# Performance work log

Measured on AMD Instinct MI355X. Metric: run time of the kernel, lower is better.

Reference implementation:

```python
import jax, jax.numpy as jnp
from jax import lax
import numpy as np

P, K1, K2 = 8, 5, 9  # nPaths, small/large ECA kernel sizes (from nDim=1024, nPaths=8)
LN_EPS = 1e-5


def setup_inputs() -> dict:
    key = jax.random.key(0)
    ks = jax.random.split(key, 6)
    b, c, l = 16, 1024, 4096
    return {
        "x": jax.random.normal(ks[0], (b, c, l), dtype=jnp.float32),
        "conv1_w": jax.random.normal(ks[1], (P, K1), dtype=jnp.float32) * 0.3,
        "conv2_w": jax.random.normal(ks[2], (P, K2), dtype=jnp.float32) * 0.3,
        "combine_w": jax.random.normal(ks[3], (2,), dtype=jnp.float32) * 0.5,
        "combine_b": jnp.zeros((), dtype=jnp.float32),
        "ln_g": jnp.ones((P,), dtype=jnp.float32),
        "ln_b": jnp.zeros((P,), dtype=jnp.float32),
        "W1": jax.random.normal(ks[4], (P, 2 * P), dtype=jnp.float32) * 0.3,
        "b1": jnp.zeros((2 * P,), dtype=jnp.float32),
        "W2": jax.random.normal(ks[5], (2 * P, P), dtype=jnp.float32) * 0.3,
        "b2": jnp.zeros((P,), dtype=jnp.float32),
    }


def _grouped_conv(y, w):
    # y: (b, P, D) pooled per-path features; w: (P, k) one 1-ch kernel per path.
    # Equivalent to the per-path Conv1d(1,1,k, padding=(k-1)//2) loop, fused.
    k = w.shape[-1]
    pad = (k - 1) // 2
    return lax.conv_general_dilated(
        y, w[:, None, :], window_strides=(1,), padding=[(pad, pad)],
        dimension_numbers=("NCH", "OIH", "NCH"), feature_group_count=y.shape[1])


def reference(x, conv1_w, conv2_w, combine_w, combine_b, ln_g, ln_b, W1, b1, W2, b2):
    b, c, l = x.shape
    nP = conv1_w.shape[0]
    D = c // nP
    pf = x.reshape(b, nP, D, l)          # (b, P, D, l)
    y = pf.mean(-1)                      # (b, P, D) global-avg-pool over l
    y1 = _grouped_conv(y, conv1_w)       # (b, P, D)
    y2 = _grouped_conv(y, conv2_w)       # (b, P, D)
    # combine = Conv1d(2,1,1): scalar mix of the two conv outputs + bias
    attn = jax.nn.sigmoid(combine_w[0] * y1 + combine_w[1] * y2 + combine_b)
    # cross-path gating MLP on per-path mean attention
    cross = attn.mean(-1)                # (b, P)
    mu = cross.mean(-1, keepdims=True)
    var = cross.var(-1, keepdims=True)   # biased, matches torch LayerNorm
    h = (cross - mu) / jnp.sqrt(var + LN_EPS) * ln_g + ln_b
    h = jax.nn.gelu(h @ W1 + b1, approximate=False)
    gate = jax.nn.sigmoid(h @ W2 + b2)   # (b, P)
    scale = attn * gate[:, :, None]      # (b, P, D)
    out = pf * scale[..., None]          # broadcast over l
    return out.reshape(b, c, l)
```

## Files before the change

kernel.cpp:

```cpp
#include <hip/hip_runtime.h>
#include <math.h>

#define NP 8
#define ND 128
#define NC 1024
#define NL 4096
#define NB 16
#define LN_EPS 1e-5f

#define NBLK 2048
#define RPB 8

typedef float v4f __attribute__((ext_vector_type(4)));

__device__ __forceinline__ float hsum(v4f v) { return v.x + v.y + v.z + v.w; }

__device__ __forceinline__ float gelu_f(float s) {
    const float t = 0.7978845608028654f * (s + 0.044715f * s * s * s);
    const float e = expf(2.f * t);
    return 0.5f * s * (1.f + (e - 1.f) / (e + 1.f));
}

__device__ __forceinline__ void gate_math(const float* __restrict__ scross,
                                          float* __restrict__ sgate,
                                          const float* ln_g, const float* ln_b,
                                          const float* W1, const float* b1,
                                          const float* W2, const float* b2) {
    float cross[NP];
    #pragma unroll
    for (int pp = 0; pp < NP; ++pp) cross[pp] = scross[pp];
    float mu = 0.f;
    #pragma unroll
    for (int pp = 0; pp < NP; ++pp) mu += cross[pp];
    mu *= (1.f / NP);
    float var = 0.f;
    #pragma unroll
    for (int pp = 0; pp < NP; ++pp) { float dl = cross[pp] - mu; var += dl * dl; }
    var *= (1.f / NP);
    const float inv = rsqrtf(var + LN_EPS);
    float h[NP];
    #pragma unroll
    for (int pp = 0; pp < NP; ++pp)
        h[pp] = (cross[pp] - mu) * inv * ln_g[pp] + ln_b[pp];
    float h2[2 * NP];
    for (int j = 0; j < 2 * NP; ++j) {
        float s = b1[j];
        #pragma unroll
        for (int pp = 0; pp < NP; ++pp) s += h[pp] * W1[pp * (2 * NP) + j];
        h2[j] = gelu_f(s);
    }
    for (int pp = 0; pp < NP; ++pp) {
        float s = b2[pp];
        #pragma unroll
        for (int j = 0; j < 2 * NP; ++j) s += h2[j] * W2[j * NP + pp];
        sgate[pp] = 1.f / (1.f + expf(-s));
    }
}

__device__ __forceinline__ void attn_math(const float* __restrict__ sy,
                                          float* __restrict__ sattn,
                                          const float* conv1_w, const float* conv2_w,
                                          const float* combine_w, const float* combine_b,
                                          int tid) {
    #pragma unroll
    for (int k = 0; k < 4; ++k) {
        const int pos = tid + 256 * k;
        const int p = pos >> 7, d = pos & 127;
        const float* rowp = sy + p * ND;
        float c1 = 0.f;
        #pragma unroll
        for (int t = 0; t < 5; ++t) {
            int dd = d + t - 2;
            float v = (dd >= 0 && dd < ND) ? rowp[dd] : 0.f;
            c1 += conv1_w[p * 5 + t] * v;
        }
        float c2 = 0.f;
        #pragma unroll
        for (int t = 0; t < 9; ++t) {
            int dd = d + t - 4;
            float v = (dd >= 0 && dd < ND) ? rowp[dd] : 0.f;
            c2 += conv2_w[p * 9 + t] * v;
        }
        const float z = combine_w[0] * c1 + combine_w[1] * c2 + combine_b[0];
        sattn[pos] = 1.f / (1.f + expf(-z));
    }
}

#define DECL_ROW(r) v4f xr##r##_0, xr##r##_1, xr##r##_2, xr##r##_3;
#define LOAD_ROW(r) { \
    const v4f* rp = xb + (size_t)(r) * (NL / 4); \
    xr##r##_0 = rp[tid]; xr##r##_1 = rp[tid + 256]; \
    xr##r##_2 = rp[tid + 512]; xr##r##_3 = rp[tid + 768]; \
    float ps = hsum(xr##r##_0) + hsum(xr##r##_1) + hsum(xr##r##_2) + hsum(xr##r##_3); \
    ps += __shfl_down(ps, 32, 64); ps += __shfl_down(ps, 16, 64); \
    ps += __shfl_down(ps, 8, 64);  ps += __shfl_down(ps, 4, 64); \
    ps += __shfl_down(ps, 2, 64);  ps += __shfl_down(ps, 1, 64); \
    if ((tid & 63) == 0) sred[r][tid >> 6] = ps; }
#define STORE_ROW(r) { \
    const float s = sattn[cbase + (r)] * g; \
    v4f* op = ob + (size_t)(r) * (NL / 4); \
    __builtin_nontemporal_store(xr##r##_0 * s, &op[tid]); \
    __builtin_nontemporal_store(xr##r##_1 * s, &op[tid + 256]); \
    __builtin_nontemporal_store(xr##r##_2 * s, &op[tid + 512]); \
    __builtin_nontemporal_store(xr##r##_3 * s, &op[tid + 768]); }

__global__ __launch_bounds__(256, 8) void fused_kernel(
    const float* __restrict__ x, float* __restrict__ y, unsigned* __restrict__ cnt,
    const float* __restrict__ conv1_w, const float* __restrict__ conv2_w,
    const float* __restrict__ combine_w, const float* __restrict__ combine_b,
    const float* __restrict__ ln_g, const float* __restrict__ ln_b,
    const float* __restrict__ W1, const float* __restrict__ b1,
    const float* __restrict__ W2, const float* __restrict__ b2,
    float* __restrict__ out)
{
    const int tid   = threadIdx.x;
    const int row0  = blockIdx.x * RPB;
    const int b     = row0 >> 10;
    const int cbase = row0 & (NC - 1);
    const int p0    = cbase >> 7;

    __shared__ float sred[RPB][4];
    __shared__ float sy[NC];
    __shared__ float sattn[NC];
    __shared__ float scross[NP];
    __shared__ float sgate[NP];

    const v4f* xb = (const v4f*)x + (size_t)row0 * (NL / 4);
    v4f* ob       = (v4f*)out    + (size_t)row0 * (NL / 4);

    DECL_ROW(0) DECL_ROW(1) DECL_ROW(2) DECL_ROW(3)
    DECL_ROW(4) DECL_ROW(5) DECL_ROW(6) DECL_ROW(7)

    LOAD_ROW(0) LOAD_ROW(1) LOAD_ROW(2) LOAD_ROW(3)
    LOAD_ROW(4) LOAD_ROW(5) LOAD_ROW(6) LOAD_ROW(7)
    __syncthreads();
    if (tid < RPB)
        y[row0 + tid] = (sred[tid][0] + sred[tid][1] + sred[tid][2] + sred[tid][3]) * (1.f / NL);
    __threadfence();
    __syncthreads();

    if (tid == 0) {
        __hip_atomic_fetch_add(cnt, 1u, __ATOMIC_RELEASE, __HIP_MEMORY_SCOPE_AGENT);
        while (__hip_atomic_load(cnt, __ATOMIC_ACQUIRE, __HIP_MEMORY_SCOPE_AGENT) < (unsigned)NBLK)
            __builtin_amdgcn_s_sleep(2);
    }
    __syncthreads();

    #pragma unroll
    for (int k = 0; k < 4; ++k) {
        const int i = tid + 256 * k;
        sy[i] = __hip_atomic_load(&y[b * NC + i], __ATOMIC_RELAXED, __HIP_MEMORY_SCOPE_AGENT);
    }
    __syncthreads();
    attn_math(sy, sattn, conv1_w, conv2_w, combine_w, combine_b, tid);
    __syncthreads();
    if (tid < 128) {
        const int p = tid >> 4, o = (tid & 15) * 8;
        float s = 0.f;
        #pragma unroll
        for (int j = 0; j < 8; ++j) s += sattn[p * ND + o + j];
        s += __shfl_down(s, 8, 16); s += __shfl_down(s, 4, 16);
        s += __shfl_down(s, 2, 16); s += __shfl_down(s, 1, 16);
        if ((tid & 15) == 0) scross[p] = s * (1.f / ND);
    }
    __syncthreads();
    if (tid == 0) gate_math(scross, sgate, ln_g, ln_b, W1, b1, W2, b2);
    __syncthreads();

    const float g = sgate[p0];
    STORE_ROW(0) STORE_ROW(1) STORE_ROW(2) STORE_ROW(3)
    STORE_ROW(4) STORE_ROW(5) STORE_ROW(6) STORE_ROW(7)
}

__global__ __launch_bounds__(256) void pool_kernel(const float* __restrict__ x,
                                                   float* __restrict__ y) {
    const int wid  = threadIdx.x >> 6;
    const int lane = threadIdx.x & 63;
    const int row  = blockIdx.x * 4 + wid;
    const v4f* xr = (const v4f*)(x + (size_t)row * NL);
    float s = 0.f;
    #pragma unroll
    for (int i = 0; i < 16; ++i) {
        v4f v = xr[lane + i * 64];
        s += v.x + v.y + v.z + v.w;
    }
    #pragma unroll
    for (int off = 32; off; off >>= 1) s += __shfl_down(s, off, 64);
    if (lane == 0) y[row] = s * (1.f / NL);
}

__global__ __launch_bounds__(1024) void attn_kernel(
    const float* __restrict__ y,
    const float* __restrict__ conv1_w, const float* __restrict__ conv2_w,
    const float* __restrict__ combine_w, const float* __restrict__ combine_b,
    const float* __restrict__ ln_g, const float* __restrict__ ln_b,
    const float* __restrict__ W1, const float* __restrict__ b1,
    const float* __restrict__ W2, const float* __restrict__ b2,
    float* __restrict__ scale)
{
    const int b = blockIdx.x;
    const int tid = threadIdx.x;
    const int p = tid >> 7;
    const int d = tid & 127;

    __shared__ float sy[NC];
    __shared__ float sattn[NC];
    __shared__ float sred[16];
    __shared__ float sgate[NP];

    sy[tid] = y[b * NC + tid];
    __syncthreads();

    const float* rowp = sy + p * ND;
    float c1 = 0.f;
    #pragma unroll
    for (int t = 0; t < 5; ++t) {
        int dd = d + t - 2;
        float v = (dd >= 0 && dd < ND) ? rowp[dd] : 0.f;
        c1 += conv1_w[p * 5 + t] * v;
    }
    float c2 = 0.f;
    #pragma unroll
    for (int t = 0; t < 9; ++t) {
        int dd = d + t - 4;
        float v = (dd >= 0 && dd < ND) ? rowp[dd] : 0.f;
        c2 += conv2_w[p * 9 + t] * v;
    }
    const float z = combine_w[0] * c1 + combine_w[1] * c2 + combine_b[0];
    const float a = 1.f / (1.f + expf(-z));
    sattn[tid] = a;

    float r = a;
    #pragma unroll
    for (int off = 32; off; off >>= 1) r += __shfl_down(r, off, 64);
    const int lane = tid & 63, wid = tid >> 6;
    if (lane == 0) sred[wid] = r;
    __syncthreads();

    if (tid == 0) {
        float scross[NP];
        #pragma unroll
        for (int pp = 0; pp < NP; ++pp)
            scross[pp] = (sred[2 * pp] + sred[2 * pp + 1]) * (1.f / ND);
        gate_math(scross, sgate, ln_g, ln_b, W1, b1, W2, b2);
    }
    __syncthreads();

    scale[b * NC + tid] = sattn[tid] * sgate[p];
}

__global__ __launch_bounds__(256) void scale_kernel(const float* __restrict__ x,
                                                    const float* __restrict__ scale,
                                                    float* __restrict__ out) {
    const v4f* xv = (const v4f*)x;
    v4f* ov = (v4f*)out;
    const size_t n = (size_t)NB * NC * (NL / 4);
    const size_t stride = (size_t)gridDim.x * blockDim.x;
    for (size_t i = (size_t)blockIdx.x * blockDim.x + threadIdx.x; i < n; i += stride) {
        const float s = scale[i >> 10];
        v4f v = xv[i];
        v *= s;
        __builtin_nontemporal_store(v, &ov[i]);
    }
}

extern "C" void kernel_launch(void* const* d_in, const int* in_sizes, int n_in,
                              void* d_out, int out_size, void* d_ws, size_t ws_size,
                              hipStream_t stream) {
    const float* x         = (const float*)d_in[0];
    const float* conv1_w   = (const float*)d_in[1];
    const float* conv2_w   = (const float*)d_in[2];
    const float* combine_w = (const float*)d_in[3];
    const float* combine_b = (const float*)d_in[4];
    const float* ln_g      = (const float*)d_in[5];
    const float* ln_b      = (const float*)d_in[6];
    const float* W1        = (const float*)d_in[7];
    const float* b1        = (const float*)d_in[8];
    const float* W2        = (const float*)d_in[9];
    const float* b2        = (const float*)d_in[10];
    float* out = (float*)d_out;

    float* y        = (float*)d_ws;
    float* scale    = y + NB * NC;
    unsigned* cnt   = (unsigned*)scale;

    hipMemsetAsync((void*)cnt, 0, 64, stream);

    int nb = 0;
    hipOccupancyMaxActiveBlocksPerMultiprocessor(&nb, fused_kernel, 256, 0);
    if (nb >= NBLK / 256) {
        void* args[] = { (void*)&x, (void*)&y, (void*)&cnt,
                         (void*)&conv1_w, (void*)&conv2_w,
                         (void*)&combine_w, (void*)&combine_b,
                         (void*)&ln_g, (void*)&ln_b,
                         (void*)&W1, (void*)&b1, (void*)&W2, (void*)&b2,
                         (void*)&out };
        hipLaunchCooperativeKernel((const void*)fused_kernel, dim3(NBLK), dim3(256),
                                   args, 0, stream);
    } else {
        pool_kernel<<<NB * NC / 4, 256, 0, stream>>>(x, y);
        attn_kernel<<<NB, 1024, 0, stream>>>(y, conv1_w, conv2_w, combine_w, combine_b,
                                             ln_g, ln_b, W1, b1, W2, b2, scale);
        scale_kernel<<<2048, 256, 0, stream>>>(x, scale, out);
    }
}
```

Baseline: 137.1 us.

## Process rows in chunks with a hierarchical per-chunk grid barrier

The fused cooperative kernel used to load 8 rows per block into registers and wait at a single grid-wide barrier on one counter. It now processes one row per block per chunk over 8 chunks. Each chunk runs a two-level barrier: 64 group counters feed a root counter, which cuts contention on one atomic. The gate MLP is also spread across threads instead of running serially on thread 0. The trade-off is 8 barrier round-trips and 8 recomputations of the attention and gate per block instead of one, and a batch's output now waits on barriers across all chunks.

```diff
diff --git a/kernel.cpp b/kernel.cpp
--- a/kernel.cpp
+++ b/kernel.cpp
@@ -9,11 +9,13 @@
 #define LN_EPS 1e-5f
 
 #define NBLK 2048
-#define RPB 8
+#define NCHUNK 8
+#define GRPS 64
 
 typedef float v4f __attribute__((ext_vector_type(4)));
 
 __device__ __forceinline__ float hsum(v4f v) { return v.x + v.y + v.z + v.w; }
+__device__ __forceinline__ float sigmoid_f(float z) { return 1.f / (1.f + expf(-z)); }
 
 __device__ __forceinline__ float gelu_f(float s) {
     const float t = 0.7978845608028654f * (s + 0.044715f * s * s * s);
@@ -21,91 +23,9 @@
     return 0.5f * s * (1.f + (e - 1.f) / (e + 1.f));
 }
 
-__device__ __forceinline__ void gate_math(const float* __restrict__ scross,
-                                          float* __restrict__ sgate,
-                                          const float* ln_g, const float* ln_b,
-                                          const float* W1, const float* b1,
-                                          const float* W2, const float* b2) {
-    float cross[NP];
-    #pragma unroll
-    for (int pp = 0; pp < NP; ++pp) cross[pp] = scross[pp];
-    float mu = 0.f;
-    #pragma unroll
-    for (int pp = 0; pp < NP; ++pp) mu += cross[pp];
-    mu *= (1.f / NP);
-    float var = 0.f;
-    #pragma unroll
-    for (int pp = 0; pp < NP; ++pp) { float dl = cross[pp] - mu; var += dl * dl; }
-    var *= (1.f / NP);
-    const float inv = rsqrtf(var + LN_EPS);
-    float h[NP];
-    #pragma unroll
-    for (int pp = 0; pp < NP; ++pp)
-        h[pp] = (cross[pp] - mu) * inv * ln_g[pp] + ln_b[pp];
-    float h2[2 * NP];
-    for (int j = 0; j < 2 * NP; ++j) {
-        float s = b1[j];
-        #pragma unroll
-        for (int pp = 0; pp < NP; ++pp) s += h[pp] * W1[pp * (2 * NP) + j];
-        h2[j] = gelu_f(s);
-    }
-    for (int pp = 0; pp < NP; ++pp) {
-        float s = b2[pp];
-        #pragma unroll
-        for (int j = 0; j < 2 * NP; ++j) s += h2[j] * W2[j * NP + pp];
-        sgate[pp] = 1.f / (1.f + expf(-s));
-    }
-}
-
-__device__ __forceinline__ void attn_math(const float* __restrict__ sy,
-                                          float* __restrict__ sattn,
-                                          const float* conv1_w, const float* conv2_w,
-                                          const float* combine_w, const float* combine_b,
-                                          int tid) {
-    #pragma unroll
-    for (int k = 0; k < 4; ++k) {
-        const int pos = tid + 256 * k;
-        const int p = pos >> 7, d = pos & 127;
-        const float* rowp = sy + p * ND;
-        float c1 = 0.f;
-        #pragma unroll
-        for (int t = 0; t < 5; ++t) {
-            int dd = d + t - 2;
-            float v = (dd >= 0 && dd < ND) ? rowp[dd] : 0.f;
-            c1 += conv1_w[p * 5 + t] * v;
-        }
-        float c2 = 0.f;
-        #pragma unroll
-        for (int t = 0; t < 9; ++t) {
-            int dd = d + t - 4;
-            float v = (dd >= 0 && dd < ND) ? rowp[dd] : 0.f;
-            c2 += conv2_w[p * 9 + t] * v;
-        }
-        const float z = combine_w[0] * c1 + combine_w[1] * c2 + combine_b[0];
-        sattn[pos] = 1.f / (1.f + expf(-z));
-    }
-}
-
-#define DECL_ROW(r) v4f xr##r##_0, xr##r##_1, xr##r##_2, xr##r##_3;
-#define LOAD_ROW(r) { \
-    const v4f* rp = xb + (size_t)(r) * (NL / 4); \
-    xr##r##_0 = rp[tid]; xr##r##_1 = rp[tid + 256]; \
-    xr##r##_2 = rp[tid + 512]; xr##r##_3 = rp[tid + 768]; \
-    float ps = hsum(xr##r##_0) + hsum(xr##r##_1) + hsum(xr##r##_2) + hsum(xr##r##_3); \
-    ps += __shfl_down(ps, 32, 64); ps += __shfl_down(ps, 16, 64); \
-    ps += __shfl_down(ps, 8, 64);  ps += __shfl_down(ps, 4, 64); \
-    ps += __shfl_down(ps, 2, 64);  ps += __shfl_down(ps, 1, 64); \
-    if ((tid & 63) == 0) sred[r][tid >> 6] = ps; }
-#define STORE_ROW(r) { \
-    const float s = sattn[cbase + (r)] * g; \
-    v4f* op = ob + (size_t)(r) * (NL / 4); \
-    __builtin_nontemporal_store(xr##r##_0 * s, &op[tid]); \
-    __builtin_nontemporal_store(xr##r##_1 * s, &op[tid + 256]); \
-    __builtin_nontemporal_store(xr##r##_2 * s, &op[tid + 512]); \
-    __builtin_nontemporal_store(xr##r##_3 * s, &op[tid + 768]); }
-
 __global__ __launch_bounds__(256, 8) void fused_kernel(
-    const float* __restrict__ x, float* __restrict__ y, unsigned* __restrict__ cnt,
+    const float* __restrict__ x, float* __restrict__ y,
+    unsigned* __restrict__ garr, unsigned* __restrict__ root,
     const float* __restrict__ conv1_w, const float* __restrict__ conv2_w,
     const float* __restrict__ combine_w, const float* __restrict__ combine_b,
     const float* __restrict__ ln_g, const float* __restrict__ ln_b,
@@ -113,63 +33,125 @@
     const float* __restrict__ W2, const float* __restrict__ b2,
     float* __restrict__ out)
 {
-    const int tid   = threadIdx.x;
-    const int row0  = blockIdx.x * RPB;
-    const int b     = row0 >> 10;
-    const int cbase = row0 & (NC - 1);
-    const int p0    = cbase >> 7;
-
-    __shared__ float sred[RPB][4];
+    const int tid = threadIdx.x;
+    const int bid = blockIdx.x;
+    const int grp = bid >> 5;
+
+    __shared__ float sred[4];
     __shared__ float sy[NC];
     __shared__ float sattn[NC];
     __shared__ float scross[NP];
+    __shared__ float sh[NP];
+    __shared__ float sh2[2 * NP];
     __shared__ float sgate[NP];
-
-    const v4f* xb = (const v4f*)x + (size_t)row0 * (NL / 4);
-    v4f* ob       = (v4f*)out    + (size_t)row0 * (NL / 4);
-
-    DECL_ROW(0) DECL_ROW(1) DECL_ROW(2) DECL_ROW(3)
-    DECL_ROW(4) DECL_ROW(5) DECL_ROW(6) DECL_ROW(7)
-
-    LOAD_ROW(0) LOAD_ROW(1) LOAD_ROW(2) LOAD_ROW(3)
-    LOAD_ROW(4) LOAD_ROW(5) LOAD_ROW(6) LOAD_ROW(7)
-    __syncthreads();
-    if (tid < RPB)
-        y[row0 + tid] = (sred[tid][0] + sred[tid][1] + sred[tid][2] + sred[tid][3]) * (1.f / NL);
-    __threadfence();
-    __syncthreads();
-
-    if (tid == 0) {
-        __hip_atomic_fetch_add(cnt, 1u, __ATOMIC_RELEASE, __HIP_MEMORY_SCOPE_AGENT);
-        while (__hip_atomic_load(cnt, __ATOMIC_ACQUIRE, __HIP_MEMORY_SCOPE_AGENT) < (unsigned)NBLK)
-            __builtin_amdgcn_s_sleep(2);
-    }
-    __syncthreads();
-
-    #pragma unroll
-    for (int k = 0; k < 4; ++k) {
-        const int i = tid + 256 * k;
-        sy[i] = __hip_atomic_load(&y[b * NC + i], __ATOMIC_RELAXED, __HIP_MEMORY_SCOPE_AGENT);
-    }
-    __syncthreads();
-    attn_math(sy, sattn, conv1_w, conv2_w, combine_w, combine_b, tid);
-    __syncthreads();
-    if (tid < 128) {
-        const int p = tid >> 4, o = (tid & 15) * 8;
-        float s = 0.f;
-        #pragma unroll
-        for (int j = 0; j < 8; ++j) s += sattn[p * ND + o + j];
-        s += __shfl_down(s, 8, 16); s += __shfl_down(s, 4, 16);
-        s += __shfl_down(s, 2, 16); s += __shfl_down(s, 1, 16);
-        if ((tid & 15) == 0) scross[p] = s * (1.f / ND);
-    }
-    __syncthreads();
-    if (tid == 0) gate_math(scross, sgate, ln_g, ln_b, W1, b1, W2, b2);
-    __syncthreads();
-
-    const float g = sgate[p0];
-    STORE_ROW(0) STORE_ROW(1) STORE_ROW(2) STORE_ROW(3)
-    STORE_ROW(4) STORE_ROW(5) STORE_ROW(6) STORE_ROW(7)
+    __shared__ float sml[2];
+
+    for (int c = 0; c < NCHUNK; ++c) {
+        const int rowc = c * NBLK + bid;
+        const int b    = rowc >> 10;
+        const int ch0  = rowc & (NC - 1);
+        const v4f* xb  = (const v4f*)x + (size_t)rowc * (NL / 4);
+        v4f* ob        = (v4f*)out    + (size_t)rowc * (NL / 4);
+
+        v4f a0 = xb[tid], a1 = xb[tid + 256], a2 = xb[tid + 512], a3 = xb[tid + 768];
+        {
+            float ps = hsum(a0) + hsum(a1) + hsum(a2) + hsum(a3);
+            ps += __shfl_down(ps, 32, 64); ps += __shfl_down(ps, 16, 64);
+            ps += __shfl_down(ps, 8, 64);  ps += __shfl_down(ps, 4, 64);
+            ps += __shfl_down(ps, 2, 64);  ps += __shfl_down(ps, 1, 64);
+            if ((tid & 63) == 0) sred[tid >> 6] = ps;
+        }
+        __syncthreads();
+        if (tid == 0) {
+            y[rowc] = (sred[0] + sred[1] + sred[2] + sred[3]) * (1.f / NL);
+            __threadfence();
+            unsigned old = __hip_atomic_fetch_add(&garr[grp], 1u,
+                              __ATOMIC_RELEASE, __HIP_MEMORY_SCOPE_AGENT);
+            if (old == (unsigned)(c * 32 + 31))
+                __hip_atomic_fetch_add(root, 1u,
+                              __ATOMIC_RELEASE, __HIP_MEMORY_SCOPE_AGENT);
+            while (__hip_atomic_load(root, __ATOMIC_ACQUIRE,
+                                     __HIP_MEMORY_SCOPE_AGENT) < (unsigned)((c + 1) * GRPS))
+                __builtin_amdgcn_s_sleep(2);
+        }
+        __syncthreads();
+
+        const float* yb = y + b * NC;
+        #pragma unroll
+        for (int k = 0; k < 4; ++k) {
+            const int i = tid + 256 * k;
+            sy[i] = __hip_atomic_load(&yb[i], __ATOMIC_RELAXED, __HIP_MEMORY_SCOPE_AGENT);
+        }
+        __syncthreads();
+        #pragma unroll
+        for (int k = 0; k < 4; ++k) {
+            const int pos = tid + 256 * k;
+            const int p = pos >> 7, d = pos & 127;
+            const float* rowp = sy + p * ND;
+            float c1 = 0.f;
+            #pragma unroll
+            for (int t = 0; t < 5; ++t) {
+                int dd = d + t - 2;
+                float v = (dd >= 0 && dd < ND) ? rowp[dd] : 0.f;
+                c1 += conv1_w[p * 5 + t] * v;
+            }
+            float c2 = 0.f;
+            #pragma unroll
+            for (int t = 0; t < 9; ++t) {
+                int dd = d + t - 4;
+                float v = (dd >= 0 && dd < ND) ? rowp[dd] : 0.f;
+                c2 += conv2_w[p * 9 + t] * v;
+            }
+            sattn[pos] = sigmoid_f(combine_w[0] * c1 + combine_w[1] * c2 + combine_b[0]);
+        }
+        __syncthreads();
+        if (tid < 128) {
+            const int p = tid >> 4, o = (tid & 15) * 8;
+            float s = 0.f;
+            #pragma unroll
+            for (int j = 0; j < 8; ++j) s += sattn[p * ND + o + j];
+            s += __shfl_down(s, 8, 16); s += __shfl_down(s, 4, 16);
+            s += __shfl_down(s, 2, 16); s += __shfl_down(s, 1, 16);
+            if ((tid & 15) == 0) scross[p] = s * (1.f / ND);
+        }
+        __syncthreads();
+        if (tid == 0) {
+            float mu = 0.f;
+            #pragma unroll
+            for (int pp = 0; pp < NP; ++pp) mu += scross[pp];
+            mu *= (1.f / NP);
+            float var = 0.f;
+            #pragma unroll
+            for (int pp = 0; pp < NP; ++pp) { float dl = scross[pp] - mu; var += dl * dl; }
+            sml[0] = mu;
+            sml[1] = rsqrtf(var * (1.f / NP) + LN_EPS);
+        }
+        __syncthreads();
+        if (tid < NP)
+            sh[tid] = (scross[tid] - sml[0]) * sml[1] * ln_g[tid] + ln_b[tid];
+        __syncthreads();
+        if (tid < 2 * NP) {
+            float s = b1[tid];
+            #pragma unroll
+            for (int pp = 0; pp < NP; ++pp) s += sh[pp] * W1[pp * (2 * NP) + tid];
+            sh2[tid] = gelu_f(s);
+        }
+        __syncthreads();
+        if (tid < NP) {
+            float s = b2[tid];
+            #pragma unroll
+            for (int j = 0; j < 2 * NP; ++j) s += sh2[j] * W2[j * NP + tid];
+            sgate[tid] = sigmoid_f(s);
+        }
+        __syncthreads();
+
+        const float s = sattn[ch0] * sgate[ch0 >> 7];
+        __builtin_nontemporal_store(a0 * s, &ob[tid]);
+        __builtin_nontemporal_store(a1 * s, &ob[tid + 256]);
+        __builtin_nontemporal_store(a2 * s, &ob[tid + 512]);
+        __builtin_nontemporal_store(a3 * s, &ob[tid + 768]);
+        __syncthreads();
+    }
 }
 
 __global__ __launch_bounds__(256) void pool_kernel(const float* __restrict__ x,
@@ -206,7 +188,11 @@
     __shared__ float sy[NC];
     __shared__ float sattn[NC];
     __shared__ float sred[16];
+    __shared__ float scross[NP];
+    __shared__ float sh[NP];
+    __shared__ float sh2[2 * NP];
     __shared__ float sgate[NP];
+    __shared__ float sml[2];
 
     sy[tid] = y[b * NC + tid];
     __syncthreads();
@@ -226,8 +212,7 @@
         float v = (dd >= 0 && dd < ND) ? rowp[dd] : 0.f;
         c2 += conv2_w[p * 9 + t] * v;
     }
-    const float z = combine_w[0] * c1 + combine_w[1] * c2 + combine_b[0];
-    const float a = 1.f / (1.f + expf(-z));
+    const float a = sigmoid_f(combine_w[0] * c1 + combine_w[1] * c2 + combine_b[0]);
     sattn[tid] = a;
 
     float r = a;
@@ -238,11 +223,34 @@
     __syncthreads();
 
     if (tid == 0) {
-        float scross[NP];
-        #pragma unroll
-        for (int pp = 0; pp < NP; ++pp)
+        float mu = 0.f, var = 0.f;
+        #pragma unroll
+        for (int pp = 0; pp < NP; ++pp) {
             scross[pp] = (sred[2 * pp] + sred[2 * pp + 1]) * (1.f / ND);
-        gate_math(scross, sgate, ln_g, ln_b, W1, b1, W2, b2);
+            mu += scross[pp];
+        }
+        mu *= (1.f / NP);
+        #pragma unroll
+        for (int pp = 0; pp < NP; ++pp) { float dl = scross[pp] - mu; var += dl * dl; }
+        sml[0] = mu;
+        sml[1] = rsqrtf(var * (1.f / NP) + LN_EPS);
+    }
+    __syncthreads();
+    if (tid < NP)
+        sh[tid] = (scross[tid] - sml[0]) * sml[1] * ln_g[tid] + ln_b[tid];
+    __syncthreads();
+    if (tid < 2 * NP) {
+        float s = b1[tid];
+        #pragma unroll
+        for (int pp = 0; pp < NP; ++pp) s += sh[pp] * W1[pp * (2 * NP) + tid];
+        sh2[tid] = gelu_f(s);
+    }
+    __syncthreads();
+    if (tid < NP) {
+        float s = b2[tid];
+        #pragma unroll
+        for (int j = 0; j < 2 * NP; ++j) s += sh2[j] * W2[j * NP + tid];
+        sgate[tid] = sigmoid_f(s);
     }
     __syncthreads();
 
@@ -282,14 +290,15 @@
 
     float* y        = (float*)d_ws;
     float* scale    = y + NB * NC;
-    unsigned* cnt   = (unsigned*)scale;
-
-    hipMemsetAsync((void*)cnt, 0, 64, stream);
+    unsigned* garr  = (unsigned*)(void*)(((char*)d_ws) + (NB * NC) * sizeof(float));
+    unsigned* root  = garr + GRPS;
+
+    hipMemsetAsync((void*)garr, 0, (GRPS + 16) * sizeof(unsigned), stream);
 
     int nb = 0;
     hipOccupancyMaxActiveBlocksPerMultiprocessor(&nb, fused_kernel, 256, 0);
     if (nb >= NBLK / 256) {
-        void* args[] = { (void*)&x, (void*)&y, (void*)&cnt,
+        void* args[] = { (void*)&x, (void*)&y, (void*)&garr, (void*)&root,
                          (void*)&conv1_w, (void*)&conv2_w,
                          (void*)&combine_w, (void*)&combine_b,
                          (void*)&ln_g, (void*)&ln_b,
```

Result: no change. 137.3 us (+0.2%).
